# Kernel tuning notes

Hardware: AMD Instinct MI355X
Metric: run time of the kernel (lower is better)

## Reference

```python
import jax, jax.numpy as jnp
import numpy as np

NC = 32          # number of cells
NDIM = 1         # 1D CPAB
NSTEPS = 32      # nstepsolver


def _expm_affine1d(A):
    """Closed-form matrix exponential of [[a, b], [0, 0]] (batched).

    A: [M, 1, 2] -> returns [M, 2, 2] with expm = [[e^a, b*phi(a)], [0, 1]],
    phi(a) = (e^a - 1)/a, with a stable small-a branch.
    """
    a = A[:, 0, 0]
    b = A[:, 0, 1]
    small = jnp.abs(a) < 1e-6
    a_safe = jnp.where(small, 1.0, a)
    phi = jnp.where(small, 1.0 + 0.5 * a, jnp.expm1(a_safe) / a_safe)
    top = jnp.stack([jnp.exp(a), b * phi], axis=-1)            # [M, 2]
    bot = jnp.broadcast_to(jnp.array([0.0, 1.0], dtype=A.dtype), top.shape)
    return jnp.stack([top, bot], axis=-2)                       # [M, 2, 2]


def setup_inputs() -> dict:
    key = jax.random.key(0)
    k1, k2, k3 = jax.random.split(key, 3)
    n_points, n_theta, d = 262144, 8, 30
    points = jax.random.uniform(k1, (NDIM, n_points), dtype=jnp.float32)
    theta = 0.5 * jax.random.normal(k2, (n_theta, d), dtype=jnp.float32)
    basis = 0.3 * jax.random.normal(k3, ((NDIM + 1) * NDIM * NC, d), dtype=jnp.float32)
    return {"points": points, "theta": theta, "basis": basis}


def reference(points, theta, basis):
    n_points = points.shape[1]
    n_theta = theta.shape[0]
    dT = 1.0 / NSTEPS

    # Per-cell affine velocity matrices: Avees [2*nC, n_theta] -> As [n_theta*nC, 1, 2]
    Avees = basis @ theta.T
    As = Avees.T.reshape(n_theta * NC, NDIM, NDIM + 1)
    Trels = _expm_affine1d(dT * As)                               # [n_theta*nC, 2, 2]

    # Repeat points per theta (theta-major flatten order, matching torch code)
    x = jnp.tile(points[0], n_theta)                              # [N]
    pts = jnp.stack([x, jnp.ones_like(x)], axis=-1)               # [N, 2] homogeneous
    batch_idx = NC * jnp.repeat(jnp.arange(n_theta, dtype=jnp.int32), n_points)

    def step(p, _):
        cell = jnp.clip(jnp.floor(p[:, 0] * NC), 0, NC - 1).astype(jnp.int32)
        T = Trels[cell + batch_idx]                               # [N, 2, 2] gather
        return jnp.einsum('nij,nj->ni', T, p), None

    pts, _ = jax.lax.scan(step, pts, None, length=NSTEPS)

    # [N, 1] -> [n_theta, ndim, n_points]
    return pts[:, :NDIM].reshape(n_theta, n_points, NDIM).transpose(0, 2, 1)
```

## Files before the change

### kernel.cpp

```cpp
#include <hip/hip_runtime.h>
#include <math.h>

#define NC 32
#define NSTEPS 32
#define NB 8192

__device__ inline void compute_tab(float* tb, const float* __restrict__ theta,
                                   const float* __restrict__ basis,
                                   int j, int d, int tid) {
    if (tid < NC) {
        const int c = tid;
        const float* __restrict__ th = theta + j * d;
        const float* __restrict__ ba = basis + (2 * c) * d;
        const float* __restrict__ bb = basis + (2 * c + 1) * d;
        float a = 0.0f, b = 0.0f;
#pragma unroll 6
        for (int k = 0; k < d; ++k) {
            float t = th[k];
            a = fmaf(ba[k], t, a);
            b = fmaf(bb[k], t, b);
        }
        const float dT = 1.0f / (float)NSTEPS;
        a *= dT;
        b *= dT;
        float A = expf(a);
        float phi = (fabsf(a) < 1e-6f) ? (1.0f + 0.5f * a) : (expm1f(a) / a);
        tb[c]      = A;
        tb[c + NC] = 32.0f * (b * phi);
    }
}

__global__ void __launch_bounds__(256)
compose_kernel(const float* __restrict__ theta,
               const float* __restrict__ basis,
               float2* __restrict__ ST, int d) {
    __shared__ float tb[2 * NC];
    const int j  = blockIdx.x >> 5;
    const int i0 = (blockIdx.x & 31) * 256;

    compute_tab(tb, theta, basis, j, d, threadIdx.x);
    __syncthreads();

    const int i = i0 + threadIdx.x;
    float zlo = (float)i * 0.00390625f;
    float zhi = __uint_as_float(
        __float_as_uint((float)(i + 1) * 0.00390625f) - 1u);
    double Sd = 1.0, Td = 0.0;
    bool pure = true;
#pragma unroll
    for (int s = 0; s < NSTEPS; ++s) {
        float flo = fminf(fmaxf(zlo, 0.0f), 31.5f);
        float fhi = fminf(fmaxf(zhi, 0.0f), 31.5f);
        int clo = (int)flo, chi = (int)fhi;
        pure = pure && (clo == chi);
        float Al = tb[clo], Bl = tb[NC + clo];
        float Ah = tb[chi], Bh = tb[NC + chi];
        Sd *= (double)Al;
        Td = fma((double)Al, Td, (double)Bl);
        zlo = fmaf(Al, zlo, Bl);
        zhi = fmaf(Ah, zhi, Bh);
    }
    float S = (float)Sd;
    ST[j * NB + i] = make_float2(pure ? S : -S, (float)(Td * (1.0 / 32.0)));
}

constexpr int MT     = 512;
constexpr int MPTS   = 8;
constexpr int MCHUNK = MT * MPTS;

__global__ void __launch_bounds__(MT)
main_kernel(const float* __restrict__ points,
            const float* __restrict__ theta,
            const float* __restrict__ basis,
            const float2* __restrict__ ST,
            float* __restrict__ out,
            int n_points, int d) {
    __shared__ float2 st[NB];
    __shared__ unsigned short ll[MCHUNK];
    __shared__ float tb[2 * NC];
    __shared__ unsigned lcnt;

    const int bpt = n_points / MCHUNK;
    const int j = blockIdx.x / bpt;
    const int cbase = (blockIdx.x % bpt) * MCHUNK;
    const int tid = threadIdx.x;

    compute_tab(tb, theta, basis, j, d, tid);
    {
        const float4* src = (const float4*)(ST + j * NB);
        float4* dst = (float4*)st;
#pragma unroll
        for (int k = 0; k < NB / 2 / MT; ++k)
            dst[k * MT + tid] = src[k * MT + tid];
    }
    if (tid == 0) lcnt = 0;
    __syncthreads();

#pragma unroll
    for (int i = 0; i < MPTS; ++i) {
        int off = i * MT + tid;
        float x = points[cbase + off];
        float f = fminf(fmaxf(x * 8192.0f, 0.0f), 8191.5f);
        float2 t = st[(int)f];
        if (t.x > 0.0f) {
            out[j * n_points + cbase + off] = fmaf(t.x, x, t.y);
        } else {
            unsigned s = atomicAdd(&lcnt, 1u);
            ll[s] = (unsigned short)off;
        }
    }
    __syncthreads();

    unsigned n = lcnt;
    for (unsigned k = tid; k < n; k += MT) {
        int off = ll[k];
        float z = points[cbase + off] * 32.0f;
#pragma unroll
        for (int s = 0; s < NSTEPS; ++s) {
            float zc = fminf(fmaxf(z, 0.0f), 31.5f);
            int c = (int)zc;
            z = fmaf(tb[c], z, tb[NC + c]);
        }
        out[j * n_points + cbase + off] = z * 0.03125f;
    }
}

extern "C" void kernel_launch(void* const* d_in, const int* in_sizes, int n_in,
                              void* d_out, int out_size, void* d_ws, size_t ws_size,
                              hipStream_t stream) {
    const float* points = (const float*)d_in[0];
    const float* theta  = (const float*)d_in[1];
    const float* basis  = (const float*)d_in[2];

    int n_points = in_sizes[0];
    int d        = in_sizes[2] / (2 * NC);
    int n_theta  = in_sizes[1] / d;

    float2* ST = (float2*)d_ws;

    compose_kernel<<<n_theta * (NB / 256), 256, 0, stream>>>(
        theta, basis, ST, d);
    main_kernel<<<n_theta * (n_points / MCHUNK), MT, 0, stream>>>(
        points, theta, basis, ST, (float*)d_out, n_points, d);
}
```

Baseline: 72.41 us.

## Fuse compose and main kernels into one cooperative launch with grid sync

Merges the table-composition kernel and the point-mapping kernel into a single cooperative kernel. A grid-wide barrier separates the phase that builds the composed ST table from the phase that maps points. The main phase now reads the table straight from global memory instead of staging 64KB into LDS. This removes one launch and the per-block LDS staging, at the cost of a grid sync and uncached random global gathers. The grid is 512 blocks of 512 threads, and the cooperative launch needs all of them co-resident.

Measured after the change: 153.3 us. +111.7%, slower.

```diff
diff --git a/kernel.cpp b/kernel.cpp
--- a/kernel.cpp
+++ b/kernel.cpp
@@ -1,9 +1,16 @@
 #include <hip/hip_runtime.h>
+#include <hip/hip_cooperative_groups.h>
 #include <math.h>
+
+namespace cg = cooperative_groups;
 
 #define NC 32
 #define NSTEPS 32
 #define NB 8192
+
+constexpr int MT     = 512;
+constexpr int MPTS   = 8;
+constexpr int MCHUNK = MT * MPTS;
 
 __device__ inline void compute_tab(float* tb, const float* __restrict__ theta,
                                    const float* __restrict__ basis,
@@ -30,78 +37,69 @@
     }
 }
 
-__global__ void __launch_bounds__(256)
-compose_kernel(const float* __restrict__ theta,
-               const float* __restrict__ basis,
-               float2* __restrict__ ST, int d) {
+__global__ void __launch_bounds__(MT, 4)
+cpab_coop(const float* __restrict__ points,
+          const float* __restrict__ theta,
+          const float* __restrict__ basis,
+          float2* __restrict__ ST,
+          float* __restrict__ out,
+          int n_points, int d, int n_theta) {
     __shared__ float tb[2 * NC];
-    const int j  = blockIdx.x >> 5;
-    const int i0 = (blockIdx.x & 31) * 256;
+    __shared__ unsigned short ll[MCHUNK];
+    __shared__ unsigned lcnt;
 
-    compute_tab(tb, theta, basis, j, d, threadIdx.x);
-    __syncthreads();
+    const int tid = threadIdx.x;
 
-    const int i = i0 + threadIdx.x;
-    float zlo = (float)i * 0.00390625f;
-    float zhi = __uint_as_float(
-        __float_as_uint((float)(i + 1) * 0.00390625f) - 1u);
-    double Sd = 1.0, Td = 0.0;
-    bool pure = true;
+    const int total_chains = n_theta * NB;
+    const int q0 = blockIdx.x * MT;
+    if (q0 < total_chains) {
+        const int jA = q0 >> 13;
+        compute_tab(tb, theta, basis, jA, d, tid);
+        __syncthreads();
+
+        const int i = (q0 + tid) & (NB - 1);
+        float zlo = (float)i * 0.00390625f;
+        float zhi = __uint_as_float(
+            __float_as_uint((float)(i + 1) * 0.00390625f) - 1u);
+        double Sd = 1.0, Td = 0.0;
+        bool pure = true;
 #pragma unroll
-    for (int s = 0; s < NSTEPS; ++s) {
-        float flo = fminf(fmaxf(zlo, 0.0f), 31.5f);
-        float fhi = fminf(fmaxf(zhi, 0.0f), 31.5f);
-        int clo = (int)flo, chi = (int)fhi;
-        pure = pure && (clo == chi);
-        float Al = tb[clo], Bl = tb[NC + clo];
-        float Ah = tb[chi], Bh = tb[NC + chi];
-        Sd *= (double)Al;
-        Td = fma((double)Al, Td, (double)Bl);
-        zlo = fmaf(Al, zlo, Bl);
-        zhi = fmaf(Ah, zhi, Bh);
+        for (int s = 0; s < NSTEPS; ++s) {
+            float flo = fminf(fmaxf(zlo, 0.0f), 31.5f);
+            float fhi = fminf(fmaxf(zhi, 0.0f), 31.5f);
+            int clo = (int)flo, chi = (int)fhi;
+            pure = pure && (clo == chi);
+            float Al = tb[clo], Bl = tb[NC + clo];
+            float Ah = tb[chi], Bh = tb[NC + chi];
+            Sd *= (double)Al;
+            Td = fma((double)Al, Td, (double)Bl);
+            zlo = fmaf(Al, zlo, Bl);
+            zhi = fmaf(Ah, zhi, Bh);
+        }
+        float S = (float)Sd;
+        ST[jA * NB + i] = make_float2(pure ? S : -S,
+                                      (float)(Td * (1.0 / 32.0)));
+        __threadfence();
     }
-    float S = (float)Sd;
-    ST[j * NB + i] = make_float2(pure ? S : -S, (float)(Td * (1.0 / 32.0)));
-}
 
-constexpr int MT     = 512;
-constexpr int MPTS   = 8;
-constexpr int MCHUNK = MT * MPTS;
-
-__global__ void __launch_bounds__(MT)
-main_kernel(const float* __restrict__ points,
-            const float* __restrict__ theta,
-            const float* __restrict__ basis,
-            const float2* __restrict__ ST,
-            float* __restrict__ out,
-            int n_points, int d) {
-    __shared__ float2 st[NB];
-    __shared__ unsigned short ll[MCHUNK];
-    __shared__ float tb[2 * NC];
-    __shared__ unsigned lcnt;
+    cg::this_grid().sync();
 
     const int bpt = n_points / MCHUNK;
     const int j = blockIdx.x / bpt;
     const int cbase = (blockIdx.x % bpt) * MCHUNK;
-    const int tid = threadIdx.x;
 
     compute_tab(tb, theta, basis, j, d, tid);
-    {
-        const float4* src = (const float4*)(ST + j * NB);
-        float4* dst = (float4*)st;
-#pragma unroll
-        for (int k = 0; k < NB / 2 / MT; ++k)
-            dst[k * MT + tid] = src[k * MT + tid];
-    }
     if (tid == 0) lcnt = 0;
     __syncthreads();
+
+    const float2* __restrict__ stj = ST + j * NB;
 
 #pragma unroll
     for (int i = 0; i < MPTS; ++i) {
         int off = i * MT + tid;
         float x = points[cbase + off];
         float f = fminf(fmaxf(x * 8192.0f, 0.0f), 8191.5f);
-        float2 t = st[(int)f];
+        float2 t = stj[(int)f];
         if (t.x > 0.0f) {
             out[j * n_points + cbase + off] = fmaf(t.x, x, t.y);
         } else {
@@ -137,9 +135,13 @@
     int n_theta  = in_sizes[1] / d;
 
     float2* ST = (float2*)d_ws;
+    float*  out = (float*)d_out;
 
-    compose_kernel<<<n_theta * (NB / 256), 256, 0, stream>>>(
-        theta, basis, ST, d);
-    main_kernel<<<n_theta * (n_points / MCHUNK), MT, 0, stream>>>(
-        points, theta, basis, ST, (float*)d_out, n_points, d);
+    int grid = n_theta * (n_points / MCHUNK);
+
+    void* args[] = {(void*)&points, (void*)&theta, (void*)&basis,
+                    (void*)&ST, (void*)&out,
+                    (void*)&n_points, (void*)&d, (void*)&n_theta};
+    hipLaunchCooperativeKernel((void*)cpab_coop, dim3(grid), dim3(MT),
+                               args, 0, stream);
 }
```

## Gather composed maps from global memory and vectorize point loads and stores

Applied to the files above, without the earlier changes.

Stops staging the full 64KB per-theta composed-map table into LDS and gathers it directly from global memory (through L2/cache) instead. Each thread now handles 8 contiguous points with float4 loads and stores, and the block size is halved to 256. This removes the large per-block LDS copy and lifts the LDS occupancy limit. The cost is scattered global gathers instead of LDS hits, and mixed points are written twice (a provisional result, then the slow-path fix).

New measurement: 76.70 us. 1.06x slower.

```diff
diff --git a/kernel.cpp b/kernel.cpp
--- a/kernel.cpp
+++ b/kernel.cpp
@@ -64,20 +64,19 @@
     ST[j * NB + i] = make_float2(pure ? S : -S, (float)(Td * (1.0 / 32.0)));
 }
 
-constexpr int MT     = 512;
+constexpr int MT     = 256;
 constexpr int MPTS   = 8;
 constexpr int MCHUNK = MT * MPTS;
 
 __global__ void __launch_bounds__(MT)
-main_kernel(const float* __restrict__ points,
-            const float* __restrict__ theta,
-            const float* __restrict__ basis,
-            const float2* __restrict__ ST,
-            float* __restrict__ out,
-            int n_points, int d) {
-    __shared__ float2 st[NB];
+apply_kernel(const float* __restrict__ points,
+             const float* __restrict__ theta,
+             const float* __restrict__ basis,
+             const float2* __restrict__ ST,
+             float* __restrict__ out,
+             int n_points, int d) {
+    __shared__ float tb[2 * NC];
     __shared__ unsigned short ll[MCHUNK];
-    __shared__ float tb[2 * NC];
     __shared__ unsigned lcnt;
 
     const int bpt = n_points / MCHUNK;
@@ -86,28 +85,35 @@
     const int tid = threadIdx.x;
 
     compute_tab(tb, theta, basis, j, d, tid);
-    {
-        const float4* src = (const float4*)(ST + j * NB);
-        float4* dst = (float4*)st;
-#pragma unroll
-        for (int k = 0; k < NB / 2 / MT; ++k)
-            dst[k * MT + tid] = src[k * MT + tid];
-    }
     if (tid == 0) lcnt = 0;
     __syncthreads();
 
+    const float2* __restrict__ stj = ST + j * NB;
+    const int p0 = cbase + tid * MPTS;
+
+    float x[MPTS];
+    {
+        float4 v0 = *(const float4*)(points + p0);
+        float4 v1 = *(const float4*)(points + p0 + 4);
+        x[0] = v0.x; x[1] = v0.y; x[2] = v0.z; x[3] = v0.w;
+        x[4] = v1.x; x[5] = v1.y; x[6] = v1.z; x[7] = v1.w;
+    }
+
+    float r[MPTS];
 #pragma unroll
     for (int i = 0; i < MPTS; ++i) {
-        int off = i * MT + tid;
-        float x = points[cbase + off];
-        float f = fminf(fmaxf(x * 8192.0f, 0.0f), 8191.5f);
-        float2 t = st[(int)f];
-        if (t.x > 0.0f) {
-            out[j * n_points + cbase + off] = fmaf(t.x, x, t.y);
-        } else {
+        float f = fminf(fmaxf(x[i] * 8192.0f, 0.0f), 8191.5f);
+        float2 t = stj[(int)f];
+        r[i] = fmaf(t.x, x[i], t.y);
+        if (!(t.x > 0.0f)) {
             unsigned s = atomicAdd(&lcnt, 1u);
-            ll[s] = (unsigned short)off;
+            ll[s] = (unsigned short)(tid * MPTS + i);
         }
+    }
+    {
+        float* op = out + j * n_points + p0;
+        *(float4*)op       = make_float4(r[0], r[1], r[2], r[3]);
+        *(float4*)(op + 4) = make_float4(r[4], r[5], r[6], r[7]);
     }
     __syncthreads();
 
@@ -140,6 +146,6 @@
 
     compose_kernel<<<n_theta * (NB / 256), 256, 0, stream>>>(
         theta, basis, ST, d);
-    main_kernel<<<n_theta * (n_points / MCHUNK), MT, 0, stream>>>(
+    apply_kernel<<<n_theta * (n_points / MCHUNK), MT, 0, stream>>>(
         points, theta, basis, ST, (float*)d_out, n_points, d);
 }
```
